# Kernel optimization log

Measured on AMD Instinct MI355X. Metric: run time of the kernel, lower is better.

The kernel has to match this reference:

```python
import jax, jax.numpy as jnp
import numpy as np

GROUP_SIZE = 64
NUM_HEADS = 16
NUM_KV_HEADS = 4
ROPE_BASE = 10000.0


def rms_norm(x):
    eps = jnp.asarray(jnp.finfo(x.dtype).eps, x.dtype)
    return x * jax.lax.rsqrt(jnp.mean(x * x, axis=-1, keepdims=True) + eps)


def ternary_weight(w, g=GROUP_SIZE):
    # fake-quant with straight-through estimator, matching torch bf16 cast
    wb = w.astype(jnp.bfloat16)
    wg = wb.reshape(-1, g)
    scale = jnp.clip(jnp.mean(jnp.abs(wg), axis=-1, keepdims=True), 1e-8)
    q = jnp.clip(jnp.round(wg / scale), -1, 1)
    wq = (q * scale).reshape(w.shape)
    return wb + jax.lax.stop_gradient(wq - wb)


def ternary_linear(x, w):
    wt = ternary_weight(w).astype(x.dtype)
    return x @ wt.T


def apply_rotary_emb(x, cos, sin):
    half = x.shape[-1] // 2
    x1, x2 = x[..., :half], x[..., half:]
    return jnp.concatenate((x1 * cos + x2 * sin, x1 * -sin + x2 * cos), axis=-1)


def rotary_tables(seq_len, head_dim, dtype):
    inv_freq = 1.0 / (ROPE_BASE ** (jnp.arange(0, head_dim, 2, dtype=jnp.float32) / head_dim))
    freqs = jnp.outer(jnp.arange(seq_len, dtype=jnp.float32), inv_freq)  # [S, D/2]
    cos = jnp.cos(freqs)[None, :, None, :].astype(dtype)  # [1,S,1,D/2]
    sin = jnp.sin(freqs)[None, :, None, :].astype(dtype)
    return cos, sin


def setup_inputs() -> dict:
    key = jax.random.key(0)
    k1, k2, k3 = jax.random.split(key, 3)
    dim = 1024
    q_size = NUM_HEADS * (dim // NUM_HEADS)
    kv_size = NUM_KV_HEADS * (dim // NUM_HEADS)
    return {
        "x": jax.random.normal(k1, (2, 2048, dim), dtype=jnp.float32),
        "w_qkv": jax.random.normal(k2, (q_size + 2 * kv_size, dim), dtype=jnp.float32) * 0.02,
        "w_proj": jax.random.normal(k3, (dim, dim), dtype=jnp.float32) * 0.02,
        "q_gain": jnp.ones((NUM_HEADS,), dtype=jnp.float32),
    }


def reference(x, w_qkv, w_proj, q_gain):
    bsz, seqlen, dim = x.shape
    head_dim = dim // NUM_HEADS
    q_size = NUM_HEADS * head_dim
    kv_size = NUM_KV_HEADS * head_dim

    qkv = ternary_linear(x, w_qkv)
    q = qkv[..., :q_size].reshape(bsz, seqlen, NUM_HEADS, head_dim)
    k = qkv[..., q_size:q_size + kv_size].reshape(bsz, seqlen, NUM_KV_HEADS, head_dim)
    v = qkv[..., q_size + kv_size:].reshape(bsz, seqlen, NUM_KV_HEADS, head_dim)

    q, k = rms_norm(q), rms_norm(k)
    cos, sin = rotary_tables(seqlen, head_dim, q.dtype)
    q = apply_rotary_emb(q, cos, sin)
    k = apply_rotary_emb(k, cos, sin)
    q = q * q_gain.astype(q.dtype)[None, None, :, None]

    # GQA: repeat kv heads
    rep = NUM_HEADS // NUM_KV_HEADS
    kr = jnp.repeat(k, rep, axis=2)  # [B,S,H,D]
    vr = jnp.repeat(v, rep, axis=2)

    scale = 1.0 / jnp.sqrt(jnp.asarray(head_dim, q.dtype))
    scores = jnp.einsum('bqhd,bkhd->bhqk', q, kr) * scale  # [B,H,S,S]
    causal = jnp.tril(jnp.ones((seqlen, seqlen), dtype=bool))
    scores = jnp.where(causal[None, None], scores, jnp.asarray(-jnp.inf, scores.dtype))
    probs = jax.nn.softmax(scores, axis=-1)
    y = jnp.einsum('bhqk,bkhd->bqhd', probs, vr).reshape(bsz, seqlen, dim)

    # NormedTernaryLinear: rms_norm then ternary linear
    return ternary_linear(rms_norm(y), w_proj)
```

## Files before the change

kernel.cpp:

```cpp
#include <hip/hip_runtime.h>
#include <cstdint>

typedef unsigned short u16;
typedef __bf16 bf16x8 __attribute__((ext_vector_type(8)));
typedef short s16x4 __attribute__((ext_vector_type(4)));
typedef int s32x2 __attribute__((ext_vector_type(2)));
typedef float f32x4 __attribute__((ext_vector_type(4)));

__device__ __forceinline__ u16 f2bf(float f) {
    unsigned u = __float_as_uint(f);
    u = (u + 0x7fffu + ((u >> 16) & 1u)) >> 16;
    return (u16)u;
}
__device__ __forceinline__ float bf2f(u16 h) {
    return __uint_as_float(((unsigned)h) << 16);
}

__device__ __forceinline__ void glds16(const u16* g, u16* l) {
    __builtin_amdgcn_global_load_lds(
        (const __attribute__((address_space(1))) void*)g,
        (__attribute__((address_space(3))) void*)l, 16, 0, 0);
}

__device__ __forceinline__ s16x4 pack_bf4(float p0, float p1, float p2, float p3) {
    unsigned a0 = __float_as_uint(p0) + 0x8000u;
    unsigned a1 = __float_as_uint(p1) + 0x8000u;
    unsigned a2 = __float_as_uint(p2) + 0x8000u;
    unsigned a3 = __float_as_uint(p3) + 0x8000u;
    s32x2 pk = {(int)__builtin_amdgcn_perm(a1, a0, 0x07060302u),
                (int)__builtin_amdgcn_perm(a3, a2, 0x07060302u)};
    return __builtin_bit_cast(s16x4, pk);
}

#if __has_builtin(__builtin_amdgcn_mfma_f32_16x16x16bf16_1k)
#define MFMA16(a, b, c) __builtin_amdgcn_mfma_f32_16x16x16bf16_1k(a, b, c, 0, 0, 0)
#else
static __device__ __forceinline__ f32x4 mfma16_asm(s16x4 a, s16x4 b, f32x4 c) {
    asm("v_mfma_f32_16x16x16_bf16 %0, %1, %2, %0" : "+v"(c) : "v"(a), "v"(b));
    return c;
}
#define MFMA16(a, b, c) mfma16_asm(a, b, c)
#endif

__global__ __launch_bounds__(256) void prep(
    const float* __restrict__ w_qkv, const float* __restrict__ w_proj,
    const float* __restrict__ x,
    u16* __restrict__ wqkv_b, u16* __restrict__ wproj_b, u16* __restrict__ xb) {
    int bid = blockIdx.x;
    if (bid < 1280) {
        const float* w; u16* o; size_t base;
        if (bid < 768) { w = w_qkv; o = wqkv_b; base = (size_t)bid * 2048; }
        else { w = w_proj; o = wproj_b; base = (size_t)(bid - 768) * 2048; }
        size_t i = base + (size_t)threadIdx.x * 8;
        float4 A = *(const float4*)(w + i);
        float4 B = *(const float4*)(w + i + 4);
        float wf[8] = {A.x, A.y, A.z, A.w, B.x, B.y, B.z, B.w};
        float wbf[8], ab[8];
        #pragma unroll
        for (int e = 0; e < 8; ++e) { wbf[e] = bf2f(f2bf(wf[e])); ab[e] = fabsf(wbf[e]); }
        float s = ((ab[0] + ab[1]) + (ab[2] + ab[3])) + ((ab[4] + ab[5]) + (ab[6] + ab[7]));
        s += __shfl_xor(s, 1);
        s += __shfl_xor(s, 2);
        s += __shfl_xor(s, 4);
        float scale = bf2f(f2bf(s * (1.0f / 64.0f)));
        if (scale < 1e-8f) scale = 1e-8f;
        u16 ov[8];
        #pragma unroll
        for (int e = 0; e < 8; ++e) {
            float t = bf2f(f2bf(wbf[e] / scale));
            float q = rintf(t);
            q = fminf(1.0f, fmaxf(-1.0f, q));
            float d = bf2f(f2bf(q * scale - wbf[e]));
            ov[e] = f2bf(wbf[e] + d);
        }
        *(int4*)(o + i) = *(const int4*)ov;
    } else {
        size_t i = ((size_t)(bid - 1280) * 256 + threadIdx.x) * 8;
        float4 a = *(const float4*)(x + i);
        float4 b = *(const float4*)(x + i + 4);
        u16 o[8] = {f2bf(a.x), f2bf(a.y), f2bf(a.z), f2bf(a.w),
                    f2bf(b.x), f2bf(b.y), f2bf(b.z), f2bf(b.w)};
        *(int4*)(xb + i) = *(const int4*)o;
    }
}

__global__ __launch_bounds__(256) void gemm_bt(
    const u16* __restrict__ A, const u16* __restrict__ B,
    float* __restrict__ C, int M, int N, int K) {
    __shared__ u16 As[2][128 * 32];
    __shared__ u16 Bs[2][64 * 32];
    const int tid = threadIdx.x;
    const int lane = tid & 63, w = tid >> 6;
    const int quad = lane >> 4, l16 = lane & 15;
    const int m0 = blockIdx.y * 128, n0 = blockIdx.x * 64;
    const int wm = (w >> 1) * 64, wn = (w & 1) * 32;

    const int sra = w * 16 + (lane >> 2);
    const int srb = tid >> 2;
    const int sg4 = lane & 3;

    f32x4 acc[4][2];
    f32x4 zero = {0.f, 0.f, 0.f, 0.f};
    #pragma unroll
    for (int i = 0; i < 4; ++i) { acc[i][0] = zero; acc[i][1] = zero; }

    int aoff[4], boff[2];
    #pragma unroll
    for (int mi = 0; mi < 4; ++mi) {
        int r = wm + mi * 16 + l16;
        aoff[mi] = r * 32 + (quad ^ ((r >> 1) & 3)) * 8;
    }
    #pragma unroll
    for (int ni = 0; ni < 2; ++ni) {
        int r = wn + ni * 16 + l16;
        boff[ni] = r * 32 + (quad ^ ((r >> 1) & 3)) * 8;
    }

    const int nk = K >> 5;
    #pragma unroll
    for (int i = 0; i < 2; ++i) {
        int r = sra + i * 64;
        int g = sg4 ^ ((r >> 1) & 3);
        glds16(A + (size_t)(m0 + r) * K + g * 8, &As[0][0] + (w * 16 + i * 64) * 32 + lane * 8);
    }
    {
        int g = sg4 ^ ((srb >> 1) & 3);
        glds16(B + (size_t)(n0 + srb) * K + g * 8, &Bs[0][0] + w * 512 + lane * 8);
    }
    __syncthreads();

    for (int kt = 0; kt < nk; ++kt) {
        if (kt + 1 < nk) {
            int k0 = (kt + 1) * 32, bi = (kt + 1) & 1;
            #pragma unroll
            for (int i = 0; i < 2; ++i) {
                int r = sra + i * 64;
                int g = sg4 ^ ((r >> 1) & 3);
                glds16(A + (size_t)(m0 + r) * K + k0 + g * 8, &As[bi][0] + (w * 16 + i * 64) * 32 + lane * 8);
            }
            int g = sg4 ^ ((srb >> 1) & 3);
            glds16(B + (size_t)(n0 + srb) * K + k0 + g * 8, &Bs[bi][0] + w * 512 + lane * 8);
        }
        const u16* as = &As[kt & 1][0];
        const u16* bs = &Bs[kt & 1][0];
        bf16x8 af[4], bfr[2];
        #pragma unroll
        for (int mi = 0; mi < 4; ++mi) af[mi]  = *(const bf16x8*)(as + aoff[mi]);
        #pragma unroll
        for (int ni = 0; ni < 2; ++ni) bfr[ni] = *(const bf16x8*)(bs + boff[ni]);
        #pragma unroll
        for (int mi = 0; mi < 4; ++mi)
            #pragma unroll
            for (int ni = 0; ni < 2; ++ni)
                acc[mi][ni] = __builtin_amdgcn_mfma_f32_16x16x32_bf16(af[mi], bfr[ni], acc[mi][ni], 0, 0, 0);
        __syncthreads();
    }
    #pragma unroll
    for (int mi = 0; mi < 4; ++mi)
        #pragma unroll
        for (int ni = 0; ni < 2; ++ni) {
            int rg = m0 + wm + mi * 16 + quad * 4;
            int cg = n0 + wn + ni * 16 + l16;
            float* cp = C + (size_t)rg * N + cg;
            #pragma unroll
            for (int r = 0; r < 4; ++r) cp[(size_t)r * N] = acc[mi][ni][r];
        }
}

__global__ __launch_bounds__(256) void fuse_qkv(
    const float* __restrict__ qkv, const float* __restrict__ gain,
    u16* __restrict__ Qb, u16* __restrict__ Kb, u16* __restrict__ Vt) {
    __shared__ u16 Vs[8][264];
    const int tid = threadIdx.x;
    const int lane = tid & 63, wid = tid >> 6;
    const int lh = lane >> 4, l16 = lane & 15;
    const int T0 = blockIdx.x * 8;
    const int dbase = l16 * 4;
    const bool hi = dbase >= 32;
    const int ibase = hi ? dbase - 32 : dbase;
    const float sgn = hi ? -1.0f : 1.0f;
    const float eps = 1.1920929e-7f;
    const float sc = 0.18033688011112042f;

    float invf[4];
    #pragma unroll
    for (int j = 0; j < 4; ++j)
        invf[j] = (float)(1.0 / pow(10000.0, (double)(ibase + j) / 32.0));

    #pragma unroll
    for (int i = 0; i < 2; ++i) {
        int tok = T0 + wid * 2 + i;
        int b = tok >> 11, s = tok & 2047;
        float cosv[4], sinv[4];
        #pragma unroll
        for (int j = 0; j < 4; ++j) {
            float fr = (float)s * invf[j];
            cosv[j] = __cosf(fr);
            sinv[j] = __sinf(fr);
        }
        const float* row = qkv + (size_t)tok * 1536;
        #pragma unroll
        for (int p = 0; p < 4; ++p) {
            int h = p * 4 + lh;
            float4 x = *(const float4*)(row + h * 64 + dbase);
            float ss = x.x * x.x + x.y * x.y + x.z * x.z + x.w * x.w;
            #pragma unroll
            for (int m = 1; m < 16; m <<= 1) ss += __shfl_xor(ss, m);
            float rn = 1.0f / sqrtf(ss * (1.0f / 64.0f) + eps);
            float xn0 = x.x * rn, xn1 = x.y * rn, xn2 = x.z * rn, xn3 = x.w * rn;
            float p0 = __shfl_xor(xn0, 8), p1 = __shfl_xor(xn1, 8);
            float p2 = __shfl_xor(xn2, 8), p3 = __shfl_xor(xn3, 8);
            float g = gain[h] * sc;
            u16 o[4] = {f2bf((xn0 * cosv[0] + sgn * p0 * sinv[0]) * g),
                        f2bf((xn1 * cosv[1] + sgn * p1 * sinv[1]) * g),
                        f2bf((xn2 * cosv[2] + sgn * p2 * sinv[2]) * g),
                        f2bf((xn3 * cosv[3] + sgn * p3 * sinv[3]) * g)};
            *(uint2*)(Qb + (((size_t)(b * 16 + h) * 2048 + s) * 64 + dbase)) = *(const uint2*)o;
        }
        {
            float4 x = *(const float4*)(row + 1024 + lh * 64 + dbase);
            float ss = x.x * x.x + x.y * x.y + x.z * x.z + x.w * x.w;
            #pragma unroll
            for (int m = 1; m < 16; m <<= 1) ss += __shfl_xor(ss, m);
            float rn = 1.0f / sqrtf(ss * (1.0f / 64.0f) + eps);
            float xn0 = x.x * rn, xn1 = x.y * rn, xn2 = x.z * rn, xn3 = x.w * rn;
            float p0 = __shfl_xor(xn0, 8), p1 = __shfl_xor(xn1, 8);
            float p2 = __shfl_xor(xn2, 8), p3 = __shfl_xor(xn3, 8);
            u16 o[4] = {f2bf(xn0 * cosv[0] + sgn * p0 * sinv[0]),
                        f2bf(xn1 * cosv[1] + sgn * p1 * sinv[1]),
                        f2bf(xn2 * cosv[2] + sgn * p2 * sinv[2]),
                        f2bf(xn3 * cosv[3] + sgn * p3 * sinv[3])};
            *(uint2*)(Kb + (((size_t)(b * 4 + lh) * 2048 + s) * 64 + dbase)) = *(const uint2*)o;
        }
        {
            float4 x = *(const float4*)(row + 1280 + lh * 64 + dbase);
            u16 o[4] = {f2bf(x.x), f2bf(x.y), f2bf(x.z), f2bf(x.w)};
            int sl = wid * 2 + i;
            *(uint2*)(&Vs[sl][lh * 64 + dbase]) = *(const uint2*)o;
        }
    }
    __syncthreads();
    {
        int kvh = tid >> 6, d = tid & 63;
        int b0 = T0 >> 11, s0 = T0 & 2047;
        u16 tmp[8];
        #pragma unroll
        for (int sl = 0; sl < 8; ++sl) tmp[sl] = Vs[sl][kvh * 64 + d];
        u16* dst = Vt + ((size_t)(b0 * 4 + kvh) * 64 + d) * 2048 + s0;
        *(int4*)(dst) = *(const int4*)(tmp);
    }
}

__global__ __launch_bounds__(512, 4) void attn(
    const u16* __restrict__ Qb, const u16* __restrict__ Kb,
    const u16* __restrict__ Vt, const float* __restrict__ gain,
    float* __restrict__ y, float* __restrict__ Opart, float* __restrict__ ml) {
    __shared__ u16 Ks[2][64 * 64];
    __shared__ u16 Vsh[2][64 * 64];
    const int hb = blockIdx.x;
    const int h = hb & 15, b = hb >> 4, kvh = h >> 2;
    const int yid = blockIdx.y;
    int bq, c0; bool partial;
    if (yid < 16) { bq = 15 - (yid >> 1); c0 = (yid & 1) * 16; partial = true; }
    else          { bq = 23 - yid;        c0 = 0;              partial = false; }
    const int nj = partial ? (c0 ? (2 * bq - 14) : 16) : (2 * bq + 2);
    const int q0 = bq * 128;
    const int tid = threadIdx.x, lane = tid & 63, w = tid >> 6;
    const int quad = lane >> 4, l16 = lane & 15;
    const float nM = -(12.0f * fabsf(gain[h]) + 1.0f);

    const u16* Qg = Qb + ((size_t)(b * 16 + h) * 2048 + q0) * 64;
    const u16* Kg = Kb + (size_t)(b * 4 + kvh) * 2048 * 64;
    const u16* Vg = Vt + (size_t)(b * 4 + kvh) * 64 * 2048;

    const bf16x8 qa0 = *(const bf16x8*)(Qg + (size_t)(w * 16 + l16) * 64 + quad * 8);
    const bf16x8 qa1 = *(const bf16x8*)(Qg + (size_t)(w * 16 + l16) * 64 + 32 + quad * 8);

    const int sr = tid >> 3;
    const int sg = (tid & 7) ^ (sr & 7);
    u16* kd[2] = {&Ks[0][0] + tid * 8, &Ks[1][0] + tid * 8};
    u16* vd[2] = {&Vsh[0][0] + tid * 8, &Vsh[1][0] + tid * 8};

    {
        int c = (c0 + nj - 1) * 64;
        glds16(Kg + (size_t)(c + sr) * 64 + sg * 8, kd[(nj - 1) & 1]);
        glds16(Vg + (size_t)sr * 2048 + c + sg * 8, vd[(nj - 1) & 1]);
    }
    __syncthreads();

    f32x4 o[4];
    f32x4 zero = {0.f, 0.f, 0.f, 0.f};
    #pragma unroll
    for (int t = 0; t < 4; ++t) o[t] = zero;
    float l = 0.f;

    for (int jj = nj - 1; jj >= 0; --jj) {
        if (jj > 0) {
            int c = (c0 + jj - 1) * 64;
            glds16(Kg + (size_t)(c + sr) * 64 + sg * 8, kd[(jj - 1) & 1]);
            glds16(Vg + (size_t)sr * 2048 + c + sg * 8, vd[(jj - 1) & 1]);
        }
        const u16* Kt = (jj & 1) ? &Ks[1][0] : &Ks[0][0];
        const u16* Vl = (jj & 1) ? &Vsh[1][0] : &Vsh[0][0];
        const int d = 8 * bq + w - 4 * (c0 + jj);
        if (d >= 0) {
            const int tmax = d < 3 ? d : 3;
            f32x4 st[4];
            #pragma unroll
            for (int t = 0; t < 4; ++t) {
                if (t <= tmax) {
                    int rk = t * 16 + l16;
                    bf16x8 kb0 = *(const bf16x8*)(Kt + rk * 64 + ((quad ^ (rk & 7)) * 8));
                    bf16x8 kb1 = *(const bf16x8*)(Kt + rk * 64 + (((quad + 4) ^ (rk & 7)) * 8));
                    f32x4 s = __builtin_amdgcn_mfma_f32_16x16x32_bf16(kb0, qa0, zero, 0, 0, 0);
                    s = __builtin_amdgcn_mfma_f32_16x16x32_bf16(kb1, qa1, s, 0, 0, 0);
                    if (t == d) {
                        #pragma unroll
                        for (int r = 0; r < 4; ++r)
                            if (quad * 4 + r > l16) s[r] = -1e30f;
                    }
                    st[t] = s;
                }
            }
            float rs = 0.f;
            s16x4 pf[4];
            #pragma unroll
            for (int t = 0; t < 4; ++t) {
                if (t <= tmax) {
                    float p0 = __builtin_amdgcn_exp2f(st[t][0] + nM);
                    float p1 = __builtin_amdgcn_exp2f(st[t][1] + nM);
                    float p2 = __builtin_amdgcn_exp2f(st[t][2] + nM);
                    float p3 = __builtin_amdgcn_exp2f(st[t][3] + nM);
                    rs += (p0 + p1) + (p2 + p3);
                    pf[t] = pack_bf4(p0, p1, p2, p3);
                }
            }
            rs += __shfl_xor(rs, 16);
            rs += __shfl_xor(rs, 32);
            l += rs;
            #pragma unroll
            for (int dt = 0; dt < 4; ++dt) {
                int rv = dt * 16 + l16;
                #pragma unroll
                for (int kt = 0; kt < 4; ++kt) {
                    if (kt <= tmax) {
                        int gv = 2 * kt + (quad >> 1);
                        s16x4 va = *(const s16x4*)(Vl + rv * 64 + ((gv ^ (rv & 7)) * 8) + (quad & 1) * 4);
                        o[dt] = MFMA16(va, pf[kt], o[dt]);
                    }
                }
            }
        }
        __syncthreads();
    }

    const int q = w * 16 + l16;
    if (!partial) {
        const float inv = 1.0f / l;
        const size_t row = (size_t)b * 2048 + q0 + q;
        #pragma unroll
        for (int dt = 0; dt < 4; ++dt) {
            f32x4 a = o[dt] * inv;
            *(f32x4*)(&y[row * 1024 + h * 64 + dt * 16 + quad * 4]) = a;
        }
    } else {
        const int slot = (hb * 8 + (bq - 8)) * 2 + (c0 ? 1 : 0);
        float* Op = Opart + (size_t)slot * 8192;
        #pragma unroll
        for (int dt = 0; dt < 4; ++dt)
            *(f32x4*)(Op + q * 64 + dt * 16 + quad * 4) = o[dt];
        if (quad == 0) ml[slot * 128 + q] = l;
    }
}

__global__ __launch_bounds__(256) void rmsnorm_merge(
    const float* __restrict__ y, const float* __restrict__ Opart,
    const float* __restrict__ ml, u16* __restrict__ yb) {
    __shared__ float red[4];
    const int row = blockIdx.x, tid = threadIdx.x;
    const int b = row >> 11, s = row & 2047;
    float4 v;
    if (s < 1024) {
        v = *(const float4*)(y + (size_t)row * 1024 + tid * 4);
    } else {
        const int bq = s >> 7, q = s & 127;
        const int e = tid * 4, h = e >> 6, dh = e & 63;
        const int slot = ((b * 16 + h) * 8 + (bq - 8)) * 2;
        float l0 = ml[slot * 128 + q];
        float l1 = ml[(slot + 1) * 128 + q];
        float inv = 1.0f / (l0 + l1);
        const float* P0 = Opart + (size_t)slot * 8192 + q * 64 + dh;
        f32x4 x0 = *(const f32x4*)P0;
        f32x4 x1 = *(const f32x4*)(P0 + 8192);
        f32x4 r = (x0 + x1) * inv;
        v.x = r[0]; v.y = r[1]; v.z = r[2]; v.w = r[3];
    }
    float ss = v.x * v.x + v.y * v.y + v.z * v.z + v.w * v.w;
    #pragma unroll
    for (int m = 1; m < 64; m <<= 1) ss += __shfl_xor(ss, m);
    if ((tid & 63) == 0) red[tid >> 6] = ss;
    __syncthreads();
    float tot = red[0] + red[1] + red[2] + red[3];
    float rn = 1.0f / sqrtf(tot * (1.0f / 1024.0f) + 1.1920929e-7f);
    u16 o[4] = {f2bf(v.x * rn), f2bf(v.y * rn), f2bf(v.z * rn), f2bf(v.w * rn)};
    *(uint2*)(yb + (size_t)row * 1024 + tid * 4) = *(const uint2*)o;
}

extern "C" void kernel_launch(void* const* d_in, const int* in_sizes, int n_in,
                              void* d_out, int out_size, void* d_ws, size_t ws_size,
                              hipStream_t stream) {
    const float* x      = (const float*)d_in[0];
    const float* w_qkv  = (const float*)d_in[1];
    const float* w_proj = (const float*)d_in[2];
    const float* q_gain = (const float*)d_in[3];
    float* out = (float*)d_out;
    char* ws = (char*)d_ws;

    u16*   wproj_b = (u16*)(ws);
    u16*   xb      = (u16*)(ws + 2097152);
    u16*   Qb      = (u16*)(ws + 2097152);
    u16*   yb      = (u16*)(ws + 2097152);
    u16*   wqkv_b  = (u16*)(ws + 10485760);
    u16*   Kb      = (u16*)(ws + 10485760);
    u16*   Vt      = (u16*)(ws + 12582912);
    float* qkv     = (float*)(ws + 14680064);
    float* y       = (float*)(ws + 14680064);
    float* Opart   = (float*)(ws + 31457280);
    float* mlb     = (float*)(ws + 48234496);

    prep<<<3328, 256, 0, stream>>>(w_qkv, w_proj, x, wqkv_b, wproj_b, xb);
    gemm_bt<<<dim3(24, 32), 256, 0, stream>>>(xb, wqkv_b, qkv, 4096, 1536, 1024);
    fuse_qkv<<<512, 256, 0, stream>>>(qkv, q_gain, Qb, Kb, Vt);
    attn<<<dim3(32, 24), 512, 0, stream>>>(Qb, Kb, Vt, q_gain, y, Opart, mlb);
    rmsnorm_merge<<<4096, 256, 0, stream>>>(y, Opart, mlb, yb);
    gemm_bt<<<dim3(16, 32), 256, 0, stream>>>(yb, wproj_b, out, 4096, 1024, 1024);
}
```

Baseline: 189.0 us.

## Fuse QKV GEMM epilogue with RMSNorm, RoPE, gain and V transpose

Replaces the QKV GEMM plus the separate fuse_qkv kernel with one GEMM whose 256x64 tile covers a whole head per block. The epilogue applies RMSNorm, rotary embedding and the gain, then writes bf16 Q/K directly. For V blocks it swaps the MFMA operands so the result comes out transposed into Vt. This drops the fp32 qkv round trip through memory and one kernel launch. In exchange the tile is larger with only 384 blocks, scalar 2-byte stores are scattered, and the workspace layout is reshuffled.

New measurement: 186.6 us. No clear change (-1.3%).

```diff
diff --git a/kernel.cpp b/kernel.cpp
--- a/kernel.cpp
+++ b/kernel.cpp
@@ -84,6 +84,139 @@
     }
 }
 
+__global__ __launch_bounds__(256) void gemm_qkv(
+    const u16* __restrict__ A, const u16* __restrict__ B,
+    const float* __restrict__ gain,
+    u16* __restrict__ Qb, u16* __restrict__ Kb, u16* __restrict__ Vt) {
+    __shared__ u16 As[2][256 * 32];
+    __shared__ u16 Bs[2][64 * 32];
+    const int tid = threadIdx.x;
+    const int lane = tid & 63, w = tid >> 6;
+    const int quad = lane >> 4, l16 = lane & 15;
+    const int bx = blockIdx.x, by = blockIdx.y;
+    const int n0 = bx * 64, t0 = by * 256;
+    const bool vblk = bx >= 20;
+    const int K = 1024, nk = 32;
+    const int b = by >> 3;
+
+    const int sra = w * 16 + (lane >> 2);
+    const int srb = tid >> 2;
+    const int sg4 = lane & 3;
+
+    f32x4 acc[4][4];
+    f32x4 zero = {0.f, 0.f, 0.f, 0.f};
+    #pragma unroll
+    for (int i = 0; i < 4; ++i)
+        #pragma unroll
+        for (int j = 0; j < 4; ++j) acc[i][j] = zero;
+
+    int aoff[4], boff[4];
+    #pragma unroll
+    for (int mi = 0; mi < 4; ++mi) {
+        int r = w * 64 + mi * 16 + l16;
+        aoff[mi] = r * 32 + (quad ^ ((r >> 1) & 3)) * 8;
+    }
+    #pragma unroll
+    for (int ni = 0; ni < 4; ++ni) {
+        int rb = ni * 16 + l16;
+        boff[ni] = rb * 32 + (quad ^ ((rb >> 1) & 3)) * 8;
+    }
+
+    #pragma unroll
+    for (int i = 0; i < 4; ++i) {
+        int r = sra + i * 64;
+        int g = sg4 ^ ((r >> 1) & 3);
+        glds16(A + (size_t)(t0 + r) * K + g * 8, &As[0][0] + (w * 16 + i * 64) * 32 + lane * 8);
+    }
+    {
+        int g = sg4 ^ ((srb >> 1) & 3);
+        glds16(B + (size_t)(n0 + srb) * K + g * 8, &Bs[0][0] + w * 512 + lane * 8);
+    }
+    __syncthreads();
+
+    for (int kt = 0; kt < nk; ++kt) {
+        if (kt + 1 < nk) {
+            int k0 = (kt + 1) * 32, bi = (kt + 1) & 1;
+            #pragma unroll
+            for (int i = 0; i < 4; ++i) {
+                int r = sra + i * 64;
+                int g = sg4 ^ ((r >> 1) & 3);
+                glds16(A + (size_t)(t0 + r) * K + k0 + g * 8, &As[bi][0] + (w * 16 + i * 64) * 32 + lane * 8);
+            }
+            int g = sg4 ^ ((srb >> 1) & 3);
+            glds16(B + (size_t)(n0 + srb) * K + k0 + g * 8, &Bs[bi][0] + w * 512 + lane * 8);
+        }
+        const u16* as = &As[kt & 1][0];
+        const u16* bs = &Bs[kt & 1][0];
+        bf16x8 af[4], bfr[4];
+        #pragma unroll
+        for (int mi = 0; mi < 4; ++mi) af[mi]  = *(const bf16x8*)(as + aoff[mi]);
+        #pragma unroll
+        for (int ni = 0; ni < 4; ++ni) bfr[ni] = *(const bf16x8*)(bs + boff[ni]);
+        if (!vblk) {
+            #pragma unroll
+            for (int mi = 0; mi < 4; ++mi)
+                #pragma unroll
+                for (int ni = 0; ni < 4; ++ni)
+                    acc[mi][ni] = __builtin_amdgcn_mfma_f32_16x16x32_bf16(af[mi], bfr[ni], acc[mi][ni], 0, 0, 0);
+        } else {
+            #pragma unroll
+            for (int mi = 0; mi < 4; ++mi)
+                #pragma unroll
+                for (int ni = 0; ni < 4; ++ni)
+                    acc[mi][ni] = __builtin_amdgcn_mfma_f32_16x16x32_bf16(bfr[ni], af[mi], acc[mi][ni], 0, 0, 0);
+        }
+        __syncthreads();
+    }
+
+    if (vblk) {
+        const int kv = bx - 20;
+        u16* vbase = Vt + (size_t)(b * 4 + kv) * 64 * 2048;
+        const int si = (t0 + w * 64 + l16) & 2047;
+        #pragma unroll
+        for (int mi = 0; mi < 4; ++mi)
+            #pragma unroll
+            for (int ni = 0; ni < 4; ++ni) {
+                int d = ni * 16 + quad * 4;
+                #pragma unroll
+                for (int r = 0; r < 4; ++r)
+                    vbase[(size_t)(d + r) * 2048 + si + mi * 16] = f2bf(acc[mi][ni][r]);
+            }
+    } else {
+        const bool isQ = bx < 16;
+        const float sc = 0.18033688011112042f;
+        const float g = isQ ? gain[bx] * sc : 1.0f;
+        u16* base = isQ ? (Qb + (size_t)(b * 16 + bx) * 2048 * 64)
+                        : (Kb + (size_t)(b * 4 + (bx - 16)) * 2048 * 64);
+        const float eps = 1.1920929e-7f;
+        const float invf0 = (float)(1.0 / pow(10000.0, (double)l16 / 32.0));
+        const float invf1 = (float)(1.0 / pow(10000.0, (double)(l16 + 16) / 32.0));
+        #pragma unroll
+        for (int mi = 0; mi < 4; ++mi) {
+            #pragma unroll
+            for (int r = 0; r < 4; ++r) {
+                float v0 = acc[mi][0][r], v1 = acc[mi][1][r];
+                float v2 = acc[mi][2][r], v3 = acc[mi][3][r];
+                float ssq = (v0 * v0 + v1 * v1) + (v2 * v2 + v3 * v3);
+                #pragma unroll
+                for (int m = 1; m < 16; m <<= 1) ssq += __shfl_xor(ssq, m);
+                float rn = 1.0f / sqrtf(ssq * (1.0f / 64.0f) + eps);
+                int si = (t0 + w * 64 + mi * 16 + quad * 4 + r) & 2047;
+                float a0 = (float)si * invf0, a1 = (float)si * invf1;
+                float c0 = __cosf(a0), s0 = __sinf(a0);
+                float c1 = __cosf(a1), s1 = __sinf(a1);
+                float x1a = v0 * rn, x2a = v2 * rn;
+                float x1b = v1 * rn, x2b = v3 * rn;
+                u16* row = base + (size_t)si * 64;
+                row[l16]      = f2bf((x1a * c0 + x2a * s0) * g);
+                row[l16 + 32] = f2bf((x2a * c0 - x1a * s0) * g);
+                row[l16 + 16] = f2bf((x1b * c1 + x2b * s1) * g);
+                row[l16 + 48] = f2bf((x2b * c1 - x1b * s1) * g);
+            }
+        }
+    }
+}
+
 __global__ __launch_bounds__(256) void gemm_bt(
     const u16* __restrict__ A, const u16* __restrict__ B,
     float* __restrict__ C, int M, int N, int K) {
@@ -165,90 +298,6 @@
             #pragma unroll
             for (int r = 0; r < 4; ++r) cp[(size_t)r * N] = acc[mi][ni][r];
         }
-}
-
-__global__ __launch_bounds__(256) void fuse_qkv(
-    const float* __restrict__ qkv, const float* __restrict__ gain,
-    u16* __restrict__ Qb, u16* __restrict__ Kb, u16* __restrict__ Vt) {
-    __shared__ u16 Vs[8][264];
-    const int tid = threadIdx.x;
-    const int lane = tid & 63, wid = tid >> 6;
-    const int lh = lane >> 4, l16 = lane & 15;
-    const int T0 = blockIdx.x * 8;
-    const int dbase = l16 * 4;
-    const bool hi = dbase >= 32;
-    const int ibase = hi ? dbase - 32 : dbase;
-    const float sgn = hi ? -1.0f : 1.0f;
-    const float eps = 1.1920929e-7f;
-    const float sc = 0.18033688011112042f;
-
-    float invf[4];
-    #pragma unroll
-    for (int j = 0; j < 4; ++j)
-        invf[j] = (float)(1.0 / pow(10000.0, (double)(ibase + j) / 32.0));
-
-    #pragma unroll
-    for (int i = 0; i < 2; ++i) {
-        int tok = T0 + wid * 2 + i;
-        int b = tok >> 11, s = tok & 2047;
-        float cosv[4], sinv[4];
-        #pragma unroll
-        for (int j = 0; j < 4; ++j) {
-            float fr = (float)s * invf[j];
-            cosv[j] = __cosf(fr);
-            sinv[j] = __sinf(fr);
-        }
-        const float* row = qkv + (size_t)tok * 1536;
-        #pragma unroll
-        for (int p = 0; p < 4; ++p) {
-            int h = p * 4 + lh;
-            float4 x = *(const float4*)(row + h * 64 + dbase);
-            float ss = x.x * x.x + x.y * x.y + x.z * x.z + x.w * x.w;
-            #pragma unroll
-            for (int m = 1; m < 16; m <<= 1) ss += __shfl_xor(ss, m);
-            float rn = 1.0f / sqrtf(ss * (1.0f / 64.0f) + eps);
-            float xn0 = x.x * rn, xn1 = x.y * rn, xn2 = x.z * rn, xn3 = x.w * rn;
-            float p0 = __shfl_xor(xn0, 8), p1 = __shfl_xor(xn1, 8);
-            float p2 = __shfl_xor(xn2, 8), p3 = __shfl_xor(xn3, 8);
-            float g = gain[h] * sc;
-            u16 o[4] = {f2bf((xn0 * cosv[0] + sgn * p0 * sinv[0]) * g),
-                        f2bf((xn1 * cosv[1] + sgn * p1 * sinv[1]) * g),
-                        f2bf((xn2 * cosv[2] + sgn * p2 * sinv[2]) * g),
-                        f2bf((xn3 * cosv[3] + sgn * p3 * sinv[3]) * g)};
-            *(uint2*)(Qb + (((size_t)(b * 16 + h) * 2048 + s) * 64 + dbase)) = *(const uint2*)o;
-        }
-        {
-            float4 x = *(const float4*)(row + 1024 + lh * 64 + dbase);
-            float ss = x.x * x.x + x.y * x.y + x.z * x.z + x.w * x.w;
-            #pragma unroll
-            for (int m = 1; m < 16; m <<= 1) ss += __shfl_xor(ss, m);
-            float rn = 1.0f / sqrtf(ss * (1.0f / 64.0f) + eps);
-            float xn0 = x.x * rn, xn1 = x.y * rn, xn2 = x.z * rn, xn3 = x.w * rn;
-            float p0 = __shfl_xor(xn0, 8), p1 = __shfl_xor(xn1, 8);
-            float p2 = __shfl_xor(xn2, 8), p3 = __shfl_xor(xn3, 8);
-            u16 o[4] = {f2bf(xn0 * cosv[0] + sgn * p0 * sinv[0]),
-                        f2bf(xn1 * cosv[1] + sgn * p1 * sinv[1]),
-                        f2bf(xn2 * cosv[2] + sgn * p2 * sinv[2]),
-                        f2bf(xn3 * cosv[3] + sgn * p3 * sinv[3])};
-            *(uint2*)(Kb + (((size_t)(b * 4 + lh) * 2048 + s) * 64 + dbase)) = *(const uint2*)o;
-        }
-        {
-            float4 x = *(const float4*)(row + 1280 + lh * 64 + dbase);
-            u16 o[4] = {f2bf(x.x), f2bf(x.y), f2bf(x.z), f2bf(x.w)};
-            int sl = wid * 2 + i;
-            *(uint2*)(&Vs[sl][lh * 64 + dbase]) = *(const uint2*)o;
-        }
-    }
-    __syncthreads();
-    {
-        int kvh = tid >> 6, d = tid & 63;
-        int b0 = T0 >> 11, s0 = T0 & 2047;
-        u16 tmp[8];
-        #pragma unroll
-        for (int sl = 0; sl < 8; ++sl) tmp[sl] = Vs[sl][kvh * 64 + d];
-        u16* dst = Vt + ((size_t)(b0 * 4 + kvh) * 64 + d) * 2048 + s0;
-        *(int4*)(dst) = *(const int4*)(tmp);
-    }
 }
 
 __global__ __launch_bounds__(512, 4) void attn(
@@ -418,19 +467,17 @@
 
     u16*   wproj_b = (u16*)(ws);
     u16*   xb      = (u16*)(ws + 2097152);
-    u16*   Qb      = (u16*)(ws + 2097152);
-    u16*   yb      = (u16*)(ws + 2097152);
+    float* y       = (float*)(ws + 2097152);
     u16*   wqkv_b  = (u16*)(ws + 10485760);
-    u16*   Kb      = (u16*)(ws + 10485760);
-    u16*   Vt      = (u16*)(ws + 12582912);
-    float* qkv     = (float*)(ws + 14680064);
-    float* y       = (float*)(ws + 14680064);
+    u16*   Qb      = (u16*)(ws + 18874368);
+    u16*   yb      = (u16*)(ws + 18874368);
+    u16*   Kb      = (u16*)(ws + 27262976);
+    u16*   Vt      = (u16*)(ws + 29360128);
     float* Opart   = (float*)(ws + 31457280);
     float* mlb     = (float*)(ws + 48234496);
 
     prep<<<3328, 256, 0, stream>>>(w_qkv, w_proj, x, wqkv_b, wproj_b, xb);
-    gemm_bt<<<dim3(24, 32), 256, 0, stream>>>(xb, wqkv_b, qkv, 4096, 1536, 1024);
-    fuse_qkv<<<512, 256, 0, stream>>>(qkv, q_gain, Qb, Kb, Vt);
+    gemm_qkv<<<dim3(24, 16), 256, 0, stream>>>(xb, wqkv_b, q_gain, Qb, Kb, Vt);
     attn<<<dim3(32, 24), 512, 0, stream>>>(Qb, Kb, Vt, q_gain, y, Opart, mlb);
     rmsnorm_merge<<<4096, 256, 0, stream>>>(y, Opart, mlb, yb);
     gemm_bt<<<dim3(16, 32), 256, 0, stream>>>(yb, wproj_b, out, 4096, 1024, 1024);
```
